# Performance work log

Hardware: AMD Instinct MI355X
Metric: run time of the kernel (lower is better)

## Reference

```python
import jax, jax.numpy as jnp
import numpy as np

N0, N1, N2 = 100000, 50000, 50000
E1, E2, E12 = 1600000, 1600000, 800000
D = 128


def scatter_mean(vals, idx, size):
    # torch_scatter.scatter_mean: sum / count, 0 for empty segments
    s = jax.ops.segment_sum(vals, idx, num_segments=size)
    c = jax.ops.segment_sum(jnp.ones((vals.shape[0], 1), vals.dtype), idx, num_segments=size)
    return s / jnp.maximum(c, 1.0)


def setup_inputs() -> dict:
    key = jax.random.key(0)
    ks = jax.random.split(key, 20)
    inp = {
        "x_node": jax.random.normal(ks[0], (N0, D), jnp.float32),
        "x1": jax.random.normal(ks[1], (N1, D), jnp.float32),
        "x2": jax.random.normal(ks[2], (N2, D), jnp.float32),
        "ei1_src": jax.random.randint(ks[3], (E1,), 0, N0, jnp.int32),
        "ei1_dst": jax.random.randint(ks[4], (E1,), 0, N1, jnp.int32),
        "ei2_src": jax.random.randint(ks[5], (E2,), 0, N0, jnp.int32),
        "ei2_dst": jax.random.randint(ks[6], (E2,), 0, N2, jnp.int32),
        "ei12_src": jax.random.randint(ks[7], (E12,), 0, N1, jnp.int32),
        "ei12_dst": jax.random.randint(ks[8], (E12,), 0, N2, jnp.int32),
        "ew1": jax.random.uniform(ks[9], (E1,), jnp.float32),
        "ew2": jax.random.uniform(ks[10], (E2,), jnp.float32),
    }
    # learned params (nn.Linear: y = x @ W.T + b)
    lim = 1.0 / np.sqrt(D)
    inp["W1"] = jax.random.uniform(ks[11], (D, D), jnp.float32, -lim, lim)
    inp["b1"] = jax.random.uniform(ks[12], (D,), jnp.float32, -lim, lim)
    inp["W2"] = jax.random.uniform(ks[13], (D, D), jnp.float32, -lim, lim)
    inp["b2"] = jax.random.uniform(ks[14], (D,), jnp.float32, -lim, lim)
    inp["W12"] = jax.random.uniform(ks[15], (D, D), jnp.float32, -lim, lim)
    inp["b12"] = jax.random.uniform(ks[16], (D,), jnp.float32, -lim, lim)
    xav = np.sqrt(6.0 / (3 + D))
    inp["att_vec"] = jax.random.uniform(ks[17], (3, D), jnp.float32, -xav, xav)
    return inp


def reference(x_node, x1, x2, ei1_src, ei1_dst, ei2_src, ei2_dst,
              ei12_src, ei12_dst, ew1, ew2,
              W1, b1, W2, b2, W12, b12, att_vec):
    n0 = x_node.shape[0]
    # metapath s-1-s
    msg_1 = scatter_mean(x_node[ei1_src] * ew1[:, None], ei1_dst, x1.shape[0])
    net_msg1 = (msg_1 + x1) * 0.5
    s1s = scatter_mean(net_msg1[ei1_dst], ei1_src, n0)
    s1s = jax.nn.relu(s1s @ W1.T + b1)  # dropout: eval mode -> identity

    # metapath s-2-s
    msg_2 = scatter_mean(x_node[ei2_src] * ew2[:, None], ei2_dst, x2.shape[0])
    net_msg2 = (msg_2 + x2) * 0.5
    s2s = scatter_mean(net_msg2[ei2_dst], ei2_src, n0)
    s2s = jax.nn.relu(s2s @ W2.T + b2)

    # metapath s-1-2-s
    msg_1b = scatter_mean(x_node[ei1_src] * ew1[:, None], ei1_dst, x1.shape[0])
    net_1b = (msg_1b + x1) * 0.5
    msg_2b = scatter_mean(net_1b[ei12_src], ei12_dst, x2.shape[0])
    net_2b = (msg_2b + x2) * 0.5
    s12s = scatter_mean(net_2b[ei2_dst] * ew2[:, None], ei2_src, n0)
    s12s = jax.nn.relu(s12s @ W12.T + b12)

    all_mp = jnp.stack([s1s, s2s, s12s], axis=1)  # [N0, 3, D]
    att_scores = jnp.einsum('nkd,kd->nk', all_mp, att_vec)
    att_w = jax.nn.softmax(att_scores, axis=1)
    return jnp.einsum('nkd,nk->nd', all_mp, att_w)
```

## Files before the change

### kernel.cpp

```cpp
#include <hip/hip_runtime.h>
#include <hip/hip_fp16.h>

#define D 128
#define CAP1 80
#define CAP2 56

typedef short s16x8 __attribute__((ext_vector_type(8)));
typedef float f32x4 __attribute__((ext_vector_type(4)));

struct FillJob {
    const int* key;
    const int* other;
    const float* w;
    int* pay;
    int cbase;
    int cap;
    int E, N;
};

__global__ __launch_bounds__(256) void fill_job_kernel(FillJob jb,
                                                       int* __restrict__ cursor) {
    int x = blockIdx.x & 7;
    int gb = blockIdx.x >> 3;
    int lo = (int)((long)jb.N * x / 8);
    int hi = (int)((long)jb.N * (x + 1) / 8);
    bool hasw = (jb.w != nullptr);
    long stride = (long)(gridDim.x >> 3) * 256;
    for (long e = (long)gb * 256 + threadIdx.x; e < jb.E; e += stride) {
        int key = jb.key[e];
        if (key < lo || key >= hi) continue;
        int pos = atomicAdd(&cursor[jb.cbase + key], 1);
        if (pos >= jb.cap) continue;
        int o = jb.other[e];
        int v;
        if (hasw) {
            int w15 = __float2int_rn(jb.w[e] * 32768.0f);
            w15 = w15 > 32767 ? 32767 : w15;
            v = (int)(((unsigned)o << 15) | (unsigned)w15);
        } else {
            v = o;
        }
        jb.pay[(long)key * jb.cap + pos] = v;
    }
}

__global__ void f2h_kernel(const float2* __restrict__ in, __half2* __restrict__ o,
                           long n2) {
    long i = (long)blockIdx.x * blockDim.x + threadIdx.x;
    if (i < n2) o[i] = __float22half2_rn(in[i]);
}

__global__ void wsplit_kernel(const float* __restrict__ W1,
                              const float* __restrict__ W2,
                              const float* __restrict__ W12,
                              unsigned short* __restrict__ hi,
                              unsigned short* __restrict__ lo) {
    int i = blockIdx.x * 256 + threadIdx.x;
    if (i >= 3 * D * D) return;
    int p = i >> 14, r = i & (D * D - 1);
    const float* W = p == 0 ? W1 : (p == 1 ? W2 : W12);
    float x = W[r];
    unsigned u = __float_as_uint(x);
    unsigned hb = u & 0xFFFF0000u;
    hi[i] = (unsigned short)(hb >> 16);
    float rem = x - __uint_as_float(hb);
    lo[i] = (unsigned short)(__float_as_uint(rem) >> 16);
}

__device__ __forceinline__ void acc8(float4 raw, float mul, float2 a[4]) {
    const __half2* h = (const __half2*)&raw;
#pragma unroll
    for (int k = 0; k < 4; ++k) {
        float2 f = __half22float2(h[k]);
        a[k].x = fmaf(f.x, mul, a[k].x);
        a[k].y = fmaf(f.y, mul, a[k].y);
    }
}

template <bool HASW>
__global__ __launch_bounds__(256) void aggh_kernel(
    const __half* __restrict__ vals, int vstride, const int* __restrict__ cnt,
    int cap, const int* __restrict__ pay, const float* __restrict__ xb,
    __half* __restrict__ dst, int dstride, int doff, int N) {
    int node = (int)(((long)blockIdx.x * 256 + threadIdx.x) >> 6);
    int lane = threadIdx.x & 63;
    if (node >= N) return;
    int count = cnt[node];
    int m = count < cap ? count : cap;
    long b0 = (long)node * cap;
    int grp = lane >> 4, il = lane & 15;
    float2 a[4] = {{0.f, 0.f}, {0.f, 0.f}, {0.f, 0.f}, {0.f, 0.f}};
    for (int base = 0; base < m; base += 64) {
        int rem = m - base;
        int n = rem < 64 ? rem : 64;
        int p = 0;
        if (lane < n) p = pay[b0 + base + lane];
        for (int j = 0; j < n; j += 4) {
            int jj = j + grp;
            int pj = __shfl(p, jj, 64);
            int g;
            float wt;
            if (HASW) {
                g = (int)(((unsigned)pj) >> 15);
                wt = (float)(pj & 0x7fff) * (1.0f / 32768.0f);
            } else {
                g = pj;
                wt = 1.0f;
            }
            float mul = jj < n ? wt : 0.0f;
            float4 raw = ((const float4*)(vals + (long)g * vstride))[il];
            acc8(raw, mul, a);
        }
    }
#pragma unroll
    for (int k = 0; k < 4; ++k) {
        a[k].x += __shfl_xor(a[k].x, 16, 64);
        a[k].y += __shfl_xor(a[k].y, 16, 64);
        a[k].x += __shfl_xor(a[k].x, 32, 64);
        a[k].y += __shfl_xor(a[k].y, 32, 64);
    }
    if (lane < 16) {
        float inv = 1.0f / fmaxf((float)count, 1.0f);
        const float4* xp = (const float4*)(xb + (long)node * D + il * 8);
        float4 x0 = xp[0], x1 = xp[1];
        float rx[8] = {x0.x, x0.y, x0.z, x0.w, x1.x, x1.y, x1.z, x1.w};
        __half2 h[4];
#pragma unroll
        for (int k = 0; k < 4; ++k) {
            float2 r;
            r.x = (a[k].x * inv + rx[2 * k + 0]) * 0.5f;
            r.y = (a[k].y * inv + rx[2 * k + 1]) * 0.5f;
            h[k] = __float22half2_rn(r);
        }
        *(float4*)(dst + (long)node * dstride + doff + il * 8) = *(float4*)h;
    }
}

__global__ __launch_bounds__(256) void aggf_kernel(
    const __half* __restrict__ vals, const int* __restrict__ cnt, int cap,
    const int* __restrict__ pay, float* __restrict__ out, int N) {
    int node = (int)(((long)blockIdx.x * 256 + threadIdx.x) >> 6);
    int lane = threadIdx.x & 63;
    if (node >= N) return;
    int count = cnt[node];
    int m = count < cap ? count : cap;
    long b0 = (long)node * cap;
    int grp = lane >> 4, il = lane & 15;
    float2 a[4] = {{0.f, 0.f}, {0.f, 0.f}, {0.f, 0.f}, {0.f, 0.f}};
    for (int base = 0; base < m; base += 64) {
        int rem = m - base;
        int n = rem < 64 ? rem : 64;
        int p = 0;
        if (lane < n) p = pay[b0 + base + lane];
        for (int j = 0; j < n; j += 4) {
            int jj = j + grp;
            int pj = __shfl(p, jj, 64);
            float mul = jj < n ? 1.0f : 0.0f;
            float4 raw = ((const float4*)(vals + (long)pj * D))[il];
            acc8(raw, mul, a);
        }
    }
#pragma unroll
    for (int k = 0; k < 4; ++k) {
        a[k].x += __shfl_xor(a[k].x, 16, 64);
        a[k].y += __shfl_xor(a[k].y, 16, 64);
        a[k].x += __shfl_xor(a[k].x, 32, 64);
        a[k].y += __shfl_xor(a[k].y, 32, 64);
    }
    if (lane < 16) {
        float inv = 1.0f / fmaxf((float)count, 1.0f);
        float4* op = (float4*)(out + (long)node * D + il * 8);
        float4 o0 = {a[0].x * inv, a[0].y * inv, a[1].x * inv, a[1].y * inv};
        float4 o1 = {a[2].x * inv, a[2].y * inv, a[3].x * inv, a[3].y * inv};
        op[0] = o0;
        op[1] = o1;
    }
}

__global__ __launch_bounds__(256) void agg2_kernel(
    const __half* __restrict__ combo, const int* __restrict__ cnt, int cap,
    const int* __restrict__ pay, float* __restrict__ outa,
    float* __restrict__ outb, int N) {
    int node = (int)(((long)blockIdx.x * 256 + threadIdx.x) >> 6);
    int lane = threadIdx.x & 63;
    if (node >= N) return;
    int count = cnt[node];
    int m = count < cap ? count : cap;
    long b0 = (long)node * cap;
    int grp = lane >> 5, il = lane & 31;
    float2 a[4] = {{0.f, 0.f}, {0.f, 0.f}, {0.f, 0.f}, {0.f, 0.f}};
    int p = 0;
    if (lane < m) p = pay[b0 + lane];
    for (int j = 0; j < m; j += 2) {
        int jj = j + grp;
        int pj = __shfl(p, jj, 64);
        int g = (int)(((unsigned)pj) >> 15);
        float w = (float)(pj & 0x7fff) * (1.0f / 32768.0f);
        float mul = jj < m ? (il < 16 ? 1.0f : w) : 0.0f;
        float4 raw = ((const float4*)(combo + (long)g * 256))[il];
        acc8(raw, mul, a);
    }
#pragma unroll
    for (int k = 0; k < 4; ++k) {
        a[k].x += __shfl_xor(a[k].x, 32, 64);
        a[k].y += __shfl_xor(a[k].y, 32, 64);
    }
    if (lane < 32) {
        float inv = 1.0f / fmaxf((float)count, 1.0f);
        float* o = (il < 16) ? (outa + (long)node * D + il * 8)
                             : (outb + (long)node * D + (il - 16) * 8);
        float4 o0 = {a[0].x * inv, a[0].y * inv, a[1].x * inv, a[1].y * inv};
        float4 o1 = {a[2].x * inv, a[2].y * inv, a[3].x * inv, a[3].y * inv};
        ((float4*)o)[0] = o0;
        ((float4*)o)[1] = o1;
    }
}

#define LO_OFF 32768

__device__ __forceinline__ int wswz(int r, int s) {
    return r * 256 + ((s ^ (r & 7)) << 4);
}

__global__ __launch_bounds__(512, 2) void mfma_tail_kernel(
    const float* __restrict__ pre1, const float* __restrict__ pre2,
    const float* pre3, const unsigned short* __restrict__ Whi,
    const unsigned short* __restrict__ Wlo, const float* __restrict__ b1,
    const float* __restrict__ b2, const float* __restrict__ b12,
    const float* __restrict__ att, float* out, int N) {
    __shared__ __align__(16) char wlds[2 * 128 * 256];
    int tid = threadIdx.x;
    int wv = tid >> 6, lane = tid & 63;
    int rw = lane & 15, kg = lane >> 4;
    int m0 = blockIdx.x * 128 + wv * 16;
    int mrow = m0 + rw;
    if (mrow >= N) mrow = N - 1;
    const float* PRE[3] = {pre1, pre2, pre3};
    const float* BB[3] = {b1, b2, b12};

    f32x4 acc[3][8];
#pragma unroll
    for (int p = 0; p < 3; ++p)
#pragma unroll
        for (int c = 0; c < 8; ++c) acc[p][c] = (f32x4){0.f, 0.f, 0.f, 0.f};

    for (int p = 0; p < 3; ++p) {
        const unsigned short* WH = Whi + ((long)p << 14);
        const unsigned short* WL = Wlo + ((long)p << 14);
#pragma unroll
        for (int c = 0; c < 4; ++c) {
            int idx = tid + c * 512;
            int r = idx >> 4, s = idx & 15;
            int dst = wswz(r, s);
            *(float4*)(wlds + dst) = *(const float4*)(WH + r * D + s * 8);
            *(float4*)(wlds + LO_OFF + dst) =
                *(const float4*)(WL + r * D + s * 8);
        }
        __syncthreads();

        const float* src = PRE[p] + (long)mrow * D + kg * 8;
#pragma unroll
        for (int kt = 0; kt < 4; ++kt) {
            float4 xa = *(const float4*)(src + kt * 32);
            float4 xb = *(const float4*)(src + kt * 32 + 4);
            float xs[8] = {xa.x, xa.y, xa.z, xa.w, xb.x, xb.y, xb.z, xb.w};
            s16x8 ah, al;
#pragma unroll
            for (int i = 0; i < 8; ++i) {
                unsigned u = __float_as_uint(xs[i]);
                unsigned hb = u & 0xFFFF0000u;
                ah[i] = (short)(hb >> 16);
                float rem = xs[i] - __uint_as_float(hb);
                al[i] = (short)(__float_as_uint(rem) >> 16);
            }
#pragma unroll
            for (int c = 0; c < 8; ++c) {
                const char* bp = wlds + wswz(c * 16 + rw, kt * 4 + kg);
                s16x8 bh = *(const s16x8*)bp;
                s16x8 bl = *(const s16x8*)(bp + LO_OFF);
                acc[p][c] = __builtin_amdgcn_mfma_f32_16x16x32_bf16(
                    ah, bh, acc[p][c], 0, 0, 0);
                acc[p][c] = __builtin_amdgcn_mfma_f32_16x16x32_bf16(
                    ah, bl, acc[p][c], 0, 0, 0);
                acc[p][c] = __builtin_amdgcn_mfma_f32_16x16x32_bf16(
                    al, bh, acc[p][c], 0, 0, 0);
            }
        }
        __syncthreads();
    }

    float sc[3][4] = {{0.f, 0.f, 0.f, 0.f},
                      {0.f, 0.f, 0.f, 0.f},
                      {0.f, 0.f, 0.f, 0.f}};
#pragma unroll
    for (int p = 0; p < 3; ++p) {
#pragma unroll
        for (int c = 0; c < 8; ++c) {
            float bv = BB[p][c * 16 + rw];
            float av = att[p * D + c * 16 + rw];
#pragma unroll
            for (int j = 0; j < 4; ++j) {
                float v = fmaxf(acc[p][c][j] + bv, 0.0f);
                acc[p][c][j] = v;
                sc[p][j] = fmaf(v, av, sc[p][j]);
            }
        }
    }
#pragma unroll
    for (int j = 0; j < 4; ++j) {
#pragma unroll
        for (int off = 1; off < 16; off <<= 1) {
            sc[0][j] += __shfl_xor(sc[0][j], off, 64);
            sc[1][j] += __shfl_xor(sc[1][j], off, 64);
            sc[2][j] += __shfl_xor(sc[2][j], off, 64);
        }
    }
#pragma unroll
    for (int j = 0; j < 4; ++j) {
        float s0 = sc[0][j], s1 = sc[1][j], s2 = sc[2][j];
        float mx = fmaxf(s0, fmaxf(s1, s2));
        float e0 = __expf(s0 - mx), e1 = __expf(s1 - mx), e2 = __expf(s2 - mx);
        float inv = 1.0f / (e0 + e1 + e2);
        float w0 = e0 * inv, w1 = e1 * inv, w2 = e2 * inv;
        int orow = m0 + kg * 4 + j;
        if (orow < N) {
            long ro = (long)orow * D + rw;
#pragma unroll
            for (int c = 0; c < 8; ++c) {
                out[ro + c * 16] =
                    acc[0][c][j] * w0 + acc[1][c][j] * w1 + acc[2][c][j] * w2;
            }
        }
    }
}

extern "C" void kernel_launch(void* const* d_in, const int* in_sizes, int n_in,
                              void* d_out, int out_size, void* d_ws,
                              size_t ws_size, hipStream_t stream) {
    const float* x_node = (const float*)d_in[0];
    const float* x1 = (const float*)d_in[1];
    const float* x2 = (const float*)d_in[2];
    const int* ei1_src = (const int*)d_in[3];
    const int* ei1_dst = (const int*)d_in[4];
    const int* ei2_src = (const int*)d_in[5];
    const int* ei2_dst = (const int*)d_in[6];
    const int* ei12_src = (const int*)d_in[7];
    const int* ei12_dst = (const int*)d_in[8];
    const float* ew1 = (const float*)d_in[9];
    const float* ew2 = (const float*)d_in[10];
    const float* W1 = (const float*)d_in[11];
    const float* b1 = (const float*)d_in[12];
    const float* W2 = (const float*)d_in[13];
    const float* b2 = (const float*)d_in[14];
    const float* W12 = (const float*)d_in[15];
    const float* b12 = (const float*)d_in[16];
    const float* att = (const float*)d_in[17];
    float* out = (float*)d_out;

    const int N0 = in_sizes[0] / D;
    const int N1 = in_sizes[1] / D;
    const int N2 = in_sizes[2] / D;
    const int E1 = in_sizes[3];
    const int E2 = in_sizes[5];
    const int E12 = in_sizes[7];

    float* ws = (float*)d_ws;
    size_t off = 0;
    auto A = [](size_t v) { return (v + 3) & ~(size_t)3; };

    __half* xh = (__half*)(ws + off);    off += A((size_t)N0 * D / 2);
    __half* net1h = (__half*)(ws + off); off += A((size_t)N1 * D / 2);
    __half* combo = (__half*)(ws + off); off += A((size_t)N2 * D);

    size_t pA = off;
    int* pay_d12 = (int*)(ws + off); off += A((size_t)N2 * CAP2);
    int* pay_s1 = (int*)(ws + off);  off += A((size_t)N0 * CAP2);
    size_t needA = pA + (size_t)N0 * D;
    if (off < needA) off = needA;
    float* pre2 = ws + pA;

    size_t pB = off;
    int* pay_d1 = (int*)(ws + off); off += A((size_t)N1 * CAP1);
    int* pay_d2 = (int*)(ws + off); off += A((size_t)N2 * CAP1);
    size_t needB = pB + (size_t)N0 * D;
    if (off < needB) off = needB;
    float* pre1 = ws + pB;

    int* pay_s2 = (int*)(ws + off); off += A((size_t)N0 * CAP2);
    float* pre3 = out;

    unsigned short* Whi = (unsigned short*)(ws + off); off += A((size_t)3 * D * D / 2);
    unsigned short* Wlo = (unsigned short*)(ws + off); off += A((size_t)3 * D * D / 2);

    const int NT = N1 + 2 * N2 + 2 * N0;
    int* cur = (int*)(ws + off); off += A(NT);
    const int cb_d1 = 0, cb_d2 = N1, cb_d12 = N1 + N2;
    const int cb_s1 = N1 + 2 * N2, cb_s2 = N1 + 2 * N2 + N0;

    hipMemsetAsync((void*)cur, 0, (size_t)NT * sizeof(int), stream);

    long n2 = (long)N0 * D / 2;
    f2h_kernel<<<(n2 + 255) / 256, 256, 0, stream>>>((const float2*)x_node,
                                                     (__half2*)xh, n2);
    wsplit_kernel<<<(3 * D * D + 255) / 256, 256, 0, stream>>>(W1, W2, W12,
                                                               Whi, Wlo);

    FillJob F[5] = {
        {ei1_dst, ei1_src, ew1, pay_d1, cb_d1, CAP1, E1, N1},
        {ei2_dst, ei2_src, ew2, pay_d2, cb_d2, CAP1, E2, N2},
        {ei12_dst, ei12_src, nullptr, pay_d12, cb_d12, CAP2, E12, N2},
        {ei1_src, ei1_dst, nullptr, pay_s1, cb_s1, CAP2, E1, N0},
        {ei2_src, ei2_dst, ew2, pay_s2, cb_s2, CAP2, E2, N0},
    };
    for (int j = 0; j < 5; ++j)
        fill_job_kernel<<<2048, 256, 0, stream>>>(F[j], cur);

    auto blocks = [](int n) { return (n + 3) / 4; };
    aggh_kernel<true><<<blocks(N1), 256, 0, stream>>>(
        xh, D, cur + cb_d1, CAP1, pay_d1, x1, net1h, D, 0, N1);
    aggh_kernel<true><<<blocks(N2), 256, 0, stream>>>(
        xh, D, cur + cb_d2, CAP1, pay_d2, x2, combo, 2 * D, 0, N2);
    aggh_kernel<false><<<blocks(N2), 256, 0, stream>>>(
        net1h, D, cur + cb_d12, CAP2, pay_d12, x2, combo, 2 * D, D, N2);
    aggf_kernel<<<blocks(N0), 256, 0, stream>>>(net1h, cur + cb_s1, CAP2,
                                                pay_s1, pre1, N0);
    agg2_kernel<<<blocks(N0), 256, 0, stream>>>(combo, cur + cb_s2, CAP2,
                                                pay_s2, pre2, pre3, N0);

    mfma_tail_kernel<<<(N0 + 127) / 128, 512, 0, stream>>>(
        pre1, pre2, pre3, Whi, Wlo, b1, b2, b12, att, out, N0);
}
```

Before: 928.9 us.

## Batch fill jobs into paired launches and split tail GEMM columns across waves

The five separate bucket-fill launches become three launches, each handling two jobs through blockIdx.y and using a larger x-grid, so independent fills run concurrently and launch gaps shrink. The MFMA tail kernel now gives each pair of waves one 16-row strip, with each wave computing half of the 128 output columns. Accumulator registers are halved and the grid doubles, which should raise occupancy. In exchange, partial attention scores must be combined through LDS with an extra barrier, and the weights are staged to LDS by twice as many blocks.

```diff
diff --git a/kernel.cpp b/kernel.cpp
--- a/kernel.cpp
+++ b/kernel.cpp
@@ -17,9 +17,11 @@
     int cap;
     int E, N;
 };
-
-__global__ __launch_bounds__(256) void fill_job_kernel(FillJob jb,
-                                                       int* __restrict__ cursor) {
+struct FillJobs2 { FillJob j[2]; };
+
+__global__ __launch_bounds__(256) void fill_pair_kernel(FillJobs2 J,
+                                                        int* __restrict__ cursor) {
+    FillJob jb = J.j[blockIdx.y];
     int x = blockIdx.x & 7;
     int gb = blockIdx.x >> 3;
     int lo = (int)((long)jb.N * x / 8);
@@ -231,18 +233,19 @@
     __shared__ __align__(16) char wlds[2 * 128 * 256];
     int tid = threadIdx.x;
     int wv = tid >> 6, lane = tid & 63;
+    int strip = wv >> 1, half = wv & 1;
     int rw = lane & 15, kg = lane >> 4;
-    int m0 = blockIdx.x * 128 + wv * 16;
+    int m0 = blockIdx.x * 64 + strip * 16;
     int mrow = m0 + rw;
     if (mrow >= N) mrow = N - 1;
     const float* PRE[3] = {pre1, pre2, pre3};
     const float* BB[3] = {b1, b2, b12};
 
-    f32x4 acc[3][8];
+    f32x4 acc[3][4];
 #pragma unroll
     for (int p = 0; p < 3; ++p)
 #pragma unroll
-        for (int c = 0; c < 8; ++c) acc[p][c] = (f32x4){0.f, 0.f, 0.f, 0.f};
+        for (int c = 0; c < 4; ++c) acc[p][c] = (f32x4){0.f, 0.f, 0.f, 0.f};
 
     for (int p = 0; p < 3; ++p) {
         const unsigned short* WH = Whi + ((long)p << 14);
@@ -274,8 +277,9 @@
                 al[i] = (short)(__float_as_uint(rem) >> 16);
             }
 #pragma unroll
-            for (int c = 0; c < 8; ++c) {
-                const char* bp = wlds + wswz(c * 16 + rw, kt * 4 + kg);
+            for (int c = 0; c < 4; ++c) {
+                const char* bp =
+                    wlds + wswz(half * 64 + c * 16 + rw, kt * 4 + kg);
                 s16x8 bh = *(const s16x8*)bp;
                 s16x8 bl = *(const s16x8*)(bp + LO_OFF);
                 acc[p][c] = __builtin_amdgcn_mfma_f32_16x16x32_bf16(
@@ -295,9 +299,10 @@
 #pragma unroll
     for (int p = 0; p < 3; ++p) {
 #pragma unroll
-        for (int c = 0; c < 8; ++c) {
-            float bv = BB[p][c * 16 + rw];
-            float av = att[p * D + c * 16 + rw];
+        for (int c = 0; c < 4; ++c) {
+            int col = half * 64 + c * 16 + rw;
+            float bv = BB[p][col];
+            float av = att[p * D + col];
 #pragma unroll
             for (int j = 0; j < 4; ++j) {
                 float v = fmaxf(acc[p][c][j] + bv, 0.0f);
@@ -315,18 +320,34 @@
             sc[2][j] += __shfl_xor(sc[2][j], off, 64);
         }
     }
+    float* sred = (float*)wlds;
+    if (rw == 0) {
+#pragma unroll
+        for (int p = 0; p < 3; ++p)
+#pragma unroll
+            for (int j = 0; j < 4; ++j)
+                sred[((strip * 2 + half) * 3 + p) * 16 + kg * 4 + j] = sc[p][j];
+    }
+    __syncthreads();
+
 #pragma unroll
     for (int j = 0; j < 4; ++j) {
-        float s0 = sc[0][j], s1 = sc[1][j], s2 = sc[2][j];
+        int row = kg * 4 + j;
+        float s0 = sred[((strip * 2 + 0) * 3 + 0) * 16 + row] +
+                   sred[((strip * 2 + 1) * 3 + 0) * 16 + row];
+        float s1 = sred[((strip * 2 + 0) * 3 + 1) * 16 + row] +
+                   sred[((strip * 2 + 1) * 3 + 1) * 16 + row];
+        float s2 = sred[((strip * 2 + 0) * 3 + 2) * 16 + row] +
+                   sred[((strip * 2 + 1) * 3 + 2) * 16 + row];
         float mx = fmaxf(s0, fmaxf(s1, s2));
         float e0 = __expf(s0 - mx), e1 = __expf(s1 - mx), e2 = __expf(s2 - mx);
         float inv = 1.0f / (e0 + e1 + e2);
         float w0 = e0 * inv, w1 = e1 * inv, w2 = e2 * inv;
-        int orow = m0 + kg * 4 + j;
+        int orow = m0 + row;
         if (orow < N) {
-            long ro = (long)orow * D + rw;
-#pragma unroll
-            for (int c = 0; c < 8; ++c) {
+            long ro = (long)orow * D + half * 64 + rw;
+#pragma unroll
+            for (int c = 0; c < 4; ++c) {
                 out[ro + c * 16] =
                     acc[0][c][j] * w0 + acc[1][c][j] * w1 + acc[2][c][j] * w2;
             }
@@ -405,15 +426,17 @@
     wsplit_kernel<<<(3 * D * D + 255) / 256, 256, 0, stream>>>(W1, W2, W12,
                                                                Whi, Wlo);
 
-    FillJob F[5] = {
-        {ei1_dst, ei1_src, ew1, pay_d1, cb_d1, CAP1, E1, N1},
-        {ei2_dst, ei2_src, ew2, pay_d2, cb_d2, CAP1, E2, N2},
-        {ei12_dst, ei12_src, nullptr, pay_d12, cb_d12, CAP2, E12, N2},
-        {ei1_src, ei1_dst, nullptr, pay_s1, cb_s1, CAP2, E1, N0},
-        {ei2_src, ei2_dst, ew2, pay_s2, cb_s2, CAP2, E2, N0},
-    };
-    for (int j = 0; j < 5; ++j)
-        fill_job_kernel<<<2048, 256, 0, stream>>>(F[j], cur);
+    FillJob jd1 = {ei1_dst, ei1_src, ew1, pay_d1, cb_d1, CAP1, E1, N1};
+    FillJob jd2 = {ei2_dst, ei2_src, ew2, pay_d2, cb_d2, CAP1, E2, N2};
+    FillJob jd12 = {ei12_dst, ei12_src, nullptr, pay_d12, cb_d12, CAP2, E12, N2};
+    FillJob js1 = {ei1_src, ei1_dst, nullptr, pay_s1, cb_s1, CAP2, E1, N0};
+    FillJob js2 = {ei2_src, ei2_dst, ew2, pay_s2, cb_s2, CAP2, E2, N0};
+    FillJobs2 P1 = {{jd1, jd2}};
+    FillJobs2 P2 = {{jd12, js1}};
+    FillJobs2 P3 = {{js2, js2}};
+    fill_pair_kernel<<<dim3(4096, 2), 256, 0, stream>>>(P1, cur);
+    fill_pair_kernel<<<dim3(4096, 2), 256, 0, stream>>>(P2, cur);
+    fill_pair_kernel<<<dim3(4096, 1), 256, 0, stream>>>(P3, cur);
 
     auto blocks = [](int n) { return (n + 3) / 4; };
     aggh_kernel<true><<<blocks(N1), 256, 0, stream>>>(
@@ -427,6 +450,6 @@
     agg2_kernel<<<blocks(N0), 256, 0, stream>>>(combo, cur + cb_s2, CAP2,
                                                 pay_s2, pre2, pre3, N0);
 
-    mfma_tail_kernel<<<(N0 + 127) / 128, 512, 0, stream>>>(
+    mfma_tail_kernel<<<(N0 + 63) / 64, 512, 0, stream>>>(
         pre1, pre2, pre3, Whi, Wlo, b1, b2, b12, att, out, N0);
 }
```

Result: faster. 892.6 us (-3.9%).
